# Performance work log

Measured on AMD Instinct MI355X. Metric: run time of the kernel, lower is better.

Reference implementation:

```python
import jax, jax.numpy as jnp
import numpy as np

# ---- config (mirrors init_kwargs) ----
T = 1024          # num tokens (one causal sequence)
H = 1024          # hidden_size
NQ, NK, D = 16, 4, 64   # q heads, kv heads, head_dim (GQA)
I_DENSE = 4096    # dense FFN intermediate
I_MOE = 512       # expert FFN intermediate
E, K = 8, 2       # num_experts, top_k
EPS = 1e-6
THETA = 10000.0


def setup_inputs() -> dict:
    key = jax.random.key(0)
    ks = jax.random.split(key, 20)
    rn = lambda k, shp: (jax.random.normal(k, shp, dtype=jnp.float32) * 0.02)
    QKV = (NQ + 2 * NK) * D
    return {
        "hidden_states": jax.random.normal(ks[0], (T, H), dtype=jnp.float32),
        "residual": jax.random.normal(ks[1], (T, H), dtype=jnp.float32),
        "positions": jnp.arange(T, dtype=jnp.int32),
        "ln0_w": jnp.ones((H,), jnp.float32),
        "pa0_w": jnp.ones((H,), jnp.float32),
        "ln1_w": jnp.ones((H,), jnp.float32),
        "pa1_w": jnp.ones((H,), jnp.float32),
        # attention weights (stored [in, out] so x @ W)
        "qkv0_w": rn(ks[2], (H, QKV)),
        "o0_w": rn(ks[3], (NQ * D, H)),
        "qkv1_w": rn(ks[4], (H, QKV)),
        "o1_w": rn(ks[5], (NQ * D, H)),
        # dense MLPs (merged gate_up: first half gate, second half up)
        "gu0_w": rn(ks[6], (H, 2 * I_DENSE)),
        "dn0_w": rn(ks[7], (I_DENSE, H)),
        "gu1_w": rn(ks[8], (H, 2 * I_DENSE)),
        "dn1_w": rn(ks[9], (I_DENSE, H)),
        # MoE: router gate + per-expert SwiGLU weights
        "gate_w": rn(ks[10], (H, E)),
        "w13": rn(ks[11], (E, H, 2 * I_MOE)),
        "w2": rn(ks[12], (E, I_MOE, H)),
    }


def _rmsnorm(x, w):
    v = jnp.mean(jnp.square(x.astype(jnp.float32)), axis=-1, keepdims=True)
    return (x.astype(jnp.float32) * jax.lax.rsqrt(v + EPS)).astype(x.dtype) * w


def _add_rmsnorm(x, res, w):
    # sglang fused add + RMSNorm: residual <- x + residual; out <- rmsnorm(residual)
    res = x + res
    return _rmsnorm(res, w), res


def _rope(pos, x):
    # neox-style rotary over full head_dim; x: [T, n_heads, D]
    half = D // 2
    inv_freq = 1.0 / (THETA ** (jnp.arange(half, dtype=jnp.float32) / half))
    f = pos.astype(jnp.float32)[:, None] * inv_freq            # [T, half]
    cos, sin = jnp.cos(f)[:, None, :], jnp.sin(f)[:, None, :]  # [T, 1, half]
    x1, x2 = x[..., :half], x[..., half:]
    return jnp.concatenate([x1 * cos - x2 * sin, x2 * cos + x1 * sin], axis=-1)


def _attention(pos, x, qkv_w, o_w):
    qkv = x @ qkv_w
    q = qkv[:, : NQ * D].reshape(T, NQ, D)
    k = qkv[:, NQ * D : (NQ + NK) * D].reshape(T, NK, D)
    v = qkv[:, (NQ + NK) * D :].reshape(T, NK, D)
    q, k = _rope(pos, q), _rope(pos, k)
    g = NQ // NK
    qg = q.reshape(T, NK, g, D)
    scores = jnp.einsum("tkgd,skd->kgts", qg, k) * (D ** -0.5)  # [NK,g,T,T]
    causal = jnp.tril(jnp.ones((T, T), bool))
    scores = jnp.where(causal, scores, jnp.float32(-1e30))
    p = jax.nn.softmax(scores, axis=-1)
    o = jnp.einsum("kgts,skd->tkgd", p, v).reshape(T, NQ * D)
    return o @ o_w


def _dense_mlp(x, gu_w, dn_w):
    gu = x @ gu_w
    h = jax.nn.silu(gu[:, :I_DENSE]) * gu[:, I_DENSE:]  # SiluAndMul
    return h @ dn_w


def _moe(x, gate_w, w13, w2):
    # router in fp32 (router_dtype == 'float32'), softmax, top-k, no renormalize
    logits = x.astype(jnp.float32) @ gate_w.astype(jnp.float32)  # [T, E]
    probs = jax.nn.softmax(logits, axis=-1)
    topw, topi = jax.lax.top_k(probs, K)                         # [T, K]
    rows = jnp.arange(x.shape[0])[:, None]
    combine = jnp.zeros((x.shape[0], E), jnp.float32).at[rows, topi].set(topw)
    combine = combine.astype(x.dtype)
    out = jnp.zeros_like(x)
    for e in range(E):  # fixed small expert count: grouped-GEMM reference
        g = x @ w13[e]
        h = jax.nn.silu(g[:, :I_MOE]) * g[:, I_MOE:]
        out = out + combine[:, e : e + 1] * (h @ w2[e])
    return out


def reference(hidden_states, residual, positions, ln0_w, pa0_w, ln1_w, pa1_w,
              qkv0_w, o0_w, qkv1_w, o1_w, gu0_w, dn0_w, gu1_w, dn1_w,
              gate_w, w13, w2):
    h, r = _add_rmsnorm(hidden_states, residual, ln0_w)
    h = _attention(positions, h, qkv0_w, o0_w)
    h, r = _add_rmsnorm(h, r, pa0_w)
    shortcut = _moe(h, gate_w, w13, w2)      # MoE runs on the shortcut branch
    h = _dense_mlp(h, gu0_w, dn0_w)
    h, r = _add_rmsnorm(h, r, ln1_w)
    h = _attention(positions, h, qkv1_w, o1_w)
    h, r = _add_rmsnorm(h, r, pa1_w)
    h = _dense_mlp(h, gu1_w, dn1_w)
    h = h + shortcut                          # combine shortcut MoE output
    return h, r
```

## Files before the change

kernel.cpp:

```cpp
#include <hip/hip_runtime.h>
#include <math.h>

namespace {

constexpr int kT = 1024;
constexpr int kH = 1024;
constexpr int kNQ = 16;
constexpr int kNKV = 4;
constexpr int kD = 64;
constexpr int kQKV = (kNQ + 2 * kNKV) * kD;
constexpr int kIDense = 4096;
constexpr int kIMoe = 512;
constexpr int kE = 8;
constexpr float kEps = 1e-6f;
constexpr long kTH = (long)kT * kH;

typedef __attribute__((ext_vector_type(8))) short short8;
typedef __attribute__((ext_vector_type(4))) float f32x4;

__device__ __forceinline__ ushort f2bf(float f) {
    union { float f; uint32_t u; } v; v.f = f;
    uint32_t r = (v.u + 0x7fffu + ((v.u >> 16) & 1u)) >> 16;
    return (ushort)r;
}
__device__ __forceinline__ void gload16(const void* g, void* l) {
    __builtin_amdgcn_global_load_lds(
        (const __attribute__((address_space(1))) void*)g,
        (__attribute__((address_space(3))) void*)l, 16, 0, 0);
}

__global__ __launch_bounds__(256) void add_rmsnorm_kernel(
    const float* __restrict__ xP, int nparts, const float* __restrict__ res,
    const float* __restrict__ w, float* __restrict__ h32,
    ushort* __restrict__ h16, float* __restrict__ r_out)
{
    __shared__ float red[4];
    const int t = blockIdx.x;
    const int i = threadIdx.x;
    const size_t base = (size_t)t * kH;
    float4 s = reinterpret_cast<const float4*>(res + base)[i];
    for (int p = 0; p < nparts; p++) {
        float4 a = reinterpret_cast<const float4*>(xP + p * kTH + base)[i];
        s.x += a.x; s.y += a.y; s.z += a.z; s.w += a.w;
    }
    reinterpret_cast<float4*>(r_out + base)[i] = s;
    float ss = s.x * s.x + s.y * s.y + s.z * s.z + s.w * s.w;
    #pragma unroll
    for (int off = 32; off > 0; off >>= 1) ss += __shfl_down(ss, off);
    if ((i & 63) == 0) red[i >> 6] = ss;
    __syncthreads();
    const float tot = red[0] + red[1] + red[2] + red[3];
    const float inv = rsqrtf(tot * (1.0f / kH) + kEps);
    float4 wv = reinterpret_cast<const float4*>(w)[i];
    float4 o = make_float4(s.x * inv * wv.x, s.y * inv * wv.y,
                           s.z * inv * wv.z, s.w * inv * wv.w);
    reinterpret_cast<float4*>(h32 + base)[i] = o;
    ushort4 u;
    u.x = f2bf(o.x); u.y = f2bf(o.y); u.z = f2bf(o.z); u.w = f2bf(o.w);
    reinterpret_cast<ushort4*>(h16 + base)[i] = u;
}

__global__ __launch_bounds__(256) void transpose_bf16_kernel(
    const float* __restrict__ W, ushort* __restrict__ WT,
    int R, int Cn, int ld_w, long w_z_stride, long wt_z_stride)
{
    __shared__ float tile[64 * 65];
    const int z = blockIdx.z;
    const float* Wz = W + (size_t)z * w_z_stride;
    ushort* WTz = WT + (size_t)z * wt_z_stride;
    const int r0 = blockIdx.y * 64;
    const int c0 = blockIdx.x * 64;
    const int tid = threadIdx.x;
    const int lr = tid >> 4;
    const int lc = (tid & 15) * 4;
    #pragma unroll
    for (int p = 0; p < 4; p++) {
        const int row = p * 16 + lr;
        float4 v = *reinterpret_cast<const float4*>(
            &Wz[(size_t)(r0 + row) * ld_w + c0 + lc]);
        tile[row * 65 + lc + 0] = v.x;
        tile[row * 65 + lc + 1] = v.y;
        tile[row * 65 + lc + 2] = v.z;
        tile[row * 65 + lc + 3] = v.w;
    }
    __syncthreads();
    const int ocl = tid >> 2;
    const int q = tid & 3;
    ushort u[16];
    #pragma unroll
    for (int e = 0; e < 16; e++)
        u[e] = f2bf(tile[(q * 16 + e) * 65 + ocl]);
    ushort* dst = &WTz[(size_t)(c0 + ocl) * R + r0 + q * 16];
    *reinterpret_cast<short8*>(dst) = *reinterpret_cast<short8*>(&u[0]);
    *reinterpret_cast<short8*>(dst + 8) = *reinterpret_cast<short8*>(&u[8]);
}

template <bool GATED>
__global__ __launch_bounds__(256) void mgemm_kernel(
    const ushort* __restrict__ A, const ushort* __restrict__ B,
    float* __restrict__ Cf, ushort* __restrict__ C16,
    const float* __restrict__ scale,
    int lda, int ldb, int ldc, int kc,
    int gate_off_rows, long b_z_stride, int c_z_col, int k_z_off,
    int scale_stride, long c_fstride)
{
    __shared__ __align__(16) ushort As[64 * 64];
    __shared__ __align__(16) ushort Bs[64 * 64];
    __shared__ __align__(16) ushort Us[GATED ? 64 * 64 : 8];

    const int z = blockIdx.z;
    const int gy = gridDim.y;
    const int nf = gridDim.x * gy;
    const int fid = blockIdx.x + gridDim.x * blockIdx.y;
    const int qq = nf >> 3;
    const int id2 = (fid & 7) * qq + (fid >> 3);
    const int m0 = (id2 % gy) * 64;
    const int n0 = (id2 / gy) * 64;

    const int tid = threadIdx.x;
    const ushort* Bz = B + (size_t)z * b_z_stride;
    const int k0 = z * k_z_off;

    const int arow = tid >> 3;
    const int achk = tid & 7;

    const int lane = tid & 63;
    const int wave = tid >> 6;
    const int wr = (wave >> 1) * 32;
    const int wc = (wave & 1) * 32;
    const int lrow = lane & 15;
    const int lg = lane >> 4;

    f32x4 accg[2][2] = {};
    f32x4 accu[2][2] = {};

    for (int kk0 = 0; kk0 < kc; kk0 += 64) {
        const int kbase = k0 + kk0;
        #pragma unroll
        for (int c = 0; c < 2; c++) {
            const int row = c * 32 + arow;
            const int cs = (achk + (row & 7)) & 7;
            gload16(A + (size_t)(m0 + row) * lda + kbase + cs * 8,
                    (char*)As + c * 4096 + tid * 16);
            gload16(Bz + (size_t)(n0 + row) * ldb + kbase + cs * 8,
                    (char*)Bs + c * 4096 + tid * 16);
            if constexpr (GATED)
                gload16(Bz + (size_t)(gate_off_rows + n0 + row) * ldb + kbase + cs * 8,
                        (char*)Us + c * 4096 + tid * 16);
        }
        __syncthreads();

        short8 af[2][2], bfr[2][2];
        #pragma unroll
        for (int mf = 0; mf < 2; mf++)
            #pragma unroll
            for (int kk = 0; kk < 2; kk++) {
                const int r = wr + mf * 16 + lrow;
                const int sl = ((kk * 4 + lg) - (r & 7)) & 7;
                af[mf][kk] = *reinterpret_cast<const short8*>(
                    (const char*)As + r * 128 + sl * 16);
            }
        #pragma unroll
        for (int nf2 = 0; nf2 < 2; nf2++)
            #pragma unroll
            for (int kk = 0; kk < 2; kk++) {
                const int n = wc + nf2 * 16 + lrow;
                const int sl = ((kk * 4 + lg) - (n & 7)) & 7;
                bfr[nf2][kk] = *reinterpret_cast<const short8*>(
                    (const char*)Bs + n * 128 + sl * 16);
            }
        #pragma unroll
        for (int mf = 0; mf < 2; mf++)
            #pragma unroll
            for (int nf2 = 0; nf2 < 2; nf2++)
                #pragma unroll
                for (int kk = 0; kk < 2; kk++)
                    accg[mf][nf2] = __builtin_amdgcn_mfma_f32_16x16x32_bf16(
                        af[mf][kk], bfr[nf2][kk], accg[mf][nf2], 0, 0, 0);
        if constexpr (GATED) {
            short8 uf[2][2];
            #pragma unroll
            for (int nf2 = 0; nf2 < 2; nf2++)
                #pragma unroll
                for (int kk = 0; kk < 2; kk++) {
                    const int n = wc + nf2 * 16 + lrow;
                    const int sl = ((kk * 4 + lg) - (n & 7)) & 7;
                    uf[nf2][kk] = *reinterpret_cast<const short8*>(
                        (const char*)Us + n * 128 + sl * 16);
                }
            #pragma unroll
            for (int mf = 0; mf < 2; mf++)
                #pragma unroll
                for (int nf2 = 0; nf2 < 2; nf2++)
                    #pragma unroll
                    for (int kk = 0; kk < 2; kk++)
                        accu[mf][nf2] = __builtin_amdgcn_mfma_f32_16x16x32_bf16(
                            af[mf][kk], uf[nf2][kk], accu[mf][nf2], 0, 0, 0);
        }
        __syncthreads();
    }

    const int r4 = (lane >> 4) * 4;
    const int cl = lane & 15;
    const int ccol = z * c_z_col;
    float* Cfz = Cf ? Cf + (size_t)z * c_fstride : nullptr;
    #pragma unroll
    for (int mf = 0; mf < 2; mf++) {
        #pragma unroll
        for (int nf2 = 0; nf2 < 2; nf2++) {
            #pragma unroll
            for (int j = 0; j < 4; j++) {
                const int row = m0 + wr + mf * 16 + r4 + j;
                const int col = ccol + n0 + wc + nf2 * 16 + cl;
                if constexpr (GATED) {
                    const float g = accg[mf][nf2][j];
                    const float u = accu[mf][nf2][j];
                    const float sv =
                        scale ? scale[(size_t)row * scale_stride + z] : 1.0f;
                    const float h = (g / (1.0f + __expf(-g))) * u * sv;
                    C16[(size_t)row * ldc + col] = f2bf(h);
                } else {
                    Cfz[(size_t)row * ldc + col] = accg[mf][nf2][j];
                }
            }
        }
    }
}

__global__ __launch_bounds__(256) void rope_pack_kernel(
    const float* __restrict__ qkv, const int* __restrict__ positions,
    ushort* __restrict__ Qb, ushort* __restrict__ Kb)
{
    const int t = blockIdx.x;
    const float pos = (float)positions[t];
    for (int item = threadIdx.x; item < (kNQ + kNKV) * 32; item += 256) {
        const int head = item >> 5;
        const int i = item & 31;
        const float inv_freq = powf(10000.0f, -(float)i * (1.0f / 32.0f));
        const float f = pos * inv_freq;
        float sv, cv;
        sincosf(f, &sv, &cv);
        const size_t off = (size_t)t * kQKV + head * kD;
        const float x1 = qkv[off + i];
        const float x2 = qkv[off + 32 + i];
        const float r1 = x1 * cv - x2 * sv;
        const float r2 = x2 * cv + x1 * sv;
        if (head < kNQ) {
            ushort* q = Qb + ((size_t)head * kT + t) * kD;
            q[i] = f2bf(r1 * 0.125f);
            q[i + 32] = f2bf(r2 * 0.125f);
        } else {
            ushort* k = Kb + ((size_t)(head - kNQ) * kT + t) * kD;
            k[i] = f2bf(r1);
            k[i + 32] = f2bf(r2);
        }
    }
}

__global__ __launch_bounds__(64) void gate_topk_kernel(
    const float* __restrict__ h, const float* __restrict__ gate_w,
    float* __restrict__ combine)
{
    const int t = blockIdx.x;
    const int lane = threadIdx.x;
    float acc[kE] = {};
    for (int i = lane; i < kH; i += 64) {
        const float xv = h[(size_t)t * kH + i];
        const float* gw = gate_w + (size_t)i * kE;
        #pragma unroll
        for (int e = 0; e < kE; e++) acc[e] += xv * gw[e];
    }
    #pragma unroll
    for (int e = 0; e < kE; e++) {
        #pragma unroll
        for (int off = 32; off > 0; off >>= 1) acc[e] += __shfl_down(acc[e], off);
    }
    if (lane == 0) {
        float mx = acc[0];
        #pragma unroll
        for (int e = 1; e < kE; e++) mx = fmaxf(mx, acc[e]);
        float p[kE];
        float s = 0.0f;
        #pragma unroll
        for (int e = 0; e < kE; e++) { p[e] = expf(acc[e] - mx); s += p[e]; }
        const float invs = 1.0f / s;
        #pragma unroll
        for (int e = 0; e < kE; e++) p[e] *= invs;
        int i1 = 0;
        #pragma unroll
        for (int e = 1; e < kE; e++) if (p[e] > p[i1]) i1 = e;
        int i2 = (i1 == 0) ? 1 : 0;
        #pragma unroll
        for (int e = 0; e < kE; e++) if (e != i1 && p[e] > p[i2]) i2 = e;
        float outv[kE];
        #pragma unroll
        for (int e = 0; e < kE; e++) outv[e] = 0.0f;
        outv[i1] = p[i1];
        outv[i2] = p[i2];
        #pragma unroll
        for (int e = 0; e < kE; e++) combine[(size_t)t * kE + e] = outv[e];
    }
}

__global__ __launch_bounds__(256) void attn_mfma_kernel(
    const ushort* __restrict__ Qb, const ushort* __restrict__ Kb,
    const ushort* __restrict__ Vt, ushort* __restrict__ attn_o)
{
    __shared__ __align__(16) ushort Qs[64 * 64];
    __shared__ __align__(16) ushort Ks[64 * 64];
    __shared__ __align__(16) ushort Vs[64 * 64];
    __shared__ __align__(16) ushort Ps[64 * 64];
    const int tid = threadIdx.x;
    const int qb = blockIdx.x * 64;
    const int hq = blockIdx.y;
    const int kvh = hq >> 2;
    const int lane = tid & 63;
    const int wave = tid >> 6;
    const int lrow = lane & 15;
    const int g = lane >> 4;
    const int srow = tid >> 3;
    const int sx = tid & 7;
    const ushort* Qg = Qb + ((size_t)hq * kT + qb) * kD;
    const ushort* Kg = Kb + (size_t)kvh * kT * kD;
    const ushort* Vg = Vt + (size_t)kvh * kD * kT;
    const int xr = (lrow & 7) << 4;

    #pragma unroll
    for (int c = 0; c < 2; c++) {
        const int row = c * 32 + srow;
        gload16(Qg + (size_t)row * kD + ((sx ^ (row & 7)) * 8),
                (char*)Qs + c * 4096 + tid * 16);
    }
    __syncthreads();
    short8 qf[2];
    #pragma unroll
    for (int kk = 0; kk < 2; kk++)
        qf[kk] = *reinterpret_cast<const short8*>(
            (const char*)Qs + (16 * wave + lrow) * 128 + ((kk * 64 + g * 16) ^ xr));

    f32x4 oacc[4] = {};
    float mrow = -1e30f, lsum = 0.0f;

    for (int s0 = 0; s0 <= qb; s0 += 64) {
        __syncthreads();
        #pragma unroll
        for (int c = 0; c < 2; c++) {
            const int row = c * 32 + srow;
            gload16(Kg + (size_t)(s0 + row) * kD + ((sx ^ (row & 7)) * 8),
                    (char*)Ks + c * 4096 + tid * 16);
            gload16(Vg + (size_t)row * kT + s0 + ((sx ^ (row & 7)) * 8),
                    (char*)Vs + c * 4096 + tid * 16);
        }
        __syncthreads();

        f32x4 sacc[4] = {};
        #pragma unroll
        for (int nf = 0; nf < 4; nf++) {
            #pragma unroll
            for (int kk = 0; kk < 2; kk++) {
                short8 kf = *reinterpret_cast<const short8*>(
                    (const char*)Ks + (nf * 16 + lrow) * 128 + ((kk * 64 + g * 16) ^ xr));
                sacc[nf] = __builtin_amdgcn_mfma_f32_16x16x32_bf16(
                    kf, qf[kk], sacc[nf], 0, 0, 0);
            }
        }

        const bool diag = (s0 == qb);
        float pv[16];
        float mloc = -1e30f;
        #pragma unroll
        for (int nf = 0; nf < 4; nf++)
            #pragma unroll
            for (int j = 0; j < 4; j++) {
                float s = sacc[nf][j];
                if (diag && (nf * 16 + g * 4 + j > 16 * wave + lrow)) s = -1e30f;
                pv[nf * 4 + j] = s;
                mloc = fmaxf(mloc, s);
            }
        mloc = fmaxf(mloc, __shfl_xor(mloc, 16));
        mloc = fmaxf(mloc, __shfl_xor(mloc, 32));
        const float mnew = fmaxf(mrow, mloc);
        const float alpha = __expf(mrow - mnew);
        float psum = 0.0f;
        #pragma unroll
        for (int j = 0; j < 16; j++) { pv[j] = __expf(pv[j] - mnew); psum += pv[j]; }
        psum += __shfl_xor(psum, 16);
        psum += __shfl_xor(psum, 32);
        lsum = lsum * alpha + psum;
        mrow = mnew;

        const int prow = 16 * wave + lrow;
        #pragma unroll
        for (int nf = 0; nf < 4; nf++)
            #pragma unroll
            for (int jp = 0; jp < 2; jp++) {
                uint32_t pk = (uint32_t)f2bf(pv[nf * 4 + jp * 2]) |
                              ((uint32_t)f2bf(pv[nf * 4 + jp * 2 + 1]) << 16);
                *reinterpret_cast<uint32_t*>(
                    (char*)Ps + prow * 128 + ((nf * 32 + g * 8 + jp * 4) ^ xr)) = pk;
            }

        float aj[4];
        #pragma unroll
        for (int j = 0; j < 4; j++) aj[j] = __shfl(alpha, g * 4 + j);
        #pragma unroll
        for (int nf = 0; nf < 4; nf++)
            #pragma unroll
            for (int j = 0; j < 4; j++) oacc[nf][j] *= aj[j];

        short8 paf[2];
        #pragma unroll
        for (int kk = 0; kk < 2; kk++)
            paf[kk] = *reinterpret_cast<const short8*>(
                (const char*)Ps + prow * 128 + ((kk * 64 + g * 16) ^ xr));
        #pragma unroll
        for (int nf = 0; nf < 4; nf++)
            #pragma unroll
            for (int kk = 0; kk < 2; kk++) {
                short8 vf = *reinterpret_cast<const short8*>(
                    (const char*)Vs + (nf * 16 + lrow) * 128 + ((kk * 64 + g * 16) ^ xr));
                oacc[nf] = __builtin_amdgcn_mfma_f32_16x16x32_bf16(
                    paf[kk], vf, oacc[nf], 0, 0, 0);
            }
    }

    float lj[4];
    #pragma unroll
    for (int j = 0; j < 4; j++) lj[j] = 1.0f / __shfl(lsum, g * 4 + j);
    #pragma unroll
    for (int nf = 0; nf < 4; nf++)
        #pragma unroll
        for (int j = 0; j < 4; j++) {
            const int trow = qb + 16 * wave + g * 4 + j;
            attn_o[(size_t)trow * (kNQ * kD) + hq * kD + nf * 16 + lrow] =
                f2bf(oacc[nf][j] * lj[j]);
        }
}

__global__ __launch_bounds__(256) void final_out_kernel(
    const float* __restrict__ mlpP, const float* __restrict__ scP,
    const float* __restrict__ r, float* __restrict__ out)
{
    const int i = blockIdx.x * 256 + threadIdx.x;
    float4 s = make_float4(0.f, 0.f, 0.f, 0.f);
    #pragma unroll
    for (int p = 0; p < 4; p++) {
        float4 a = reinterpret_cast<const float4*>(mlpP + p * kTH)[i];
        float4 b = reinterpret_cast<const float4*>(scP + p * kTH)[i];
        s.x += a.x + b.x; s.y += a.y + b.y; s.z += a.z + b.z; s.w += a.w + b.w;
    }
    reinterpret_cast<float4*>(out)[i] = s;
    reinterpret_cast<float4*>(out + kTH)[i] =
        reinterpret_cast<const float4*>(r)[i];
}

}

extern "C" void kernel_launch(void* const* d_in, const int* in_sizes, int n_in,
                              void* d_out, int out_size, void* d_ws, size_t ws_size,
                              hipStream_t stream) {
    (void)in_sizes; (void)n_in; (void)out_size; (void)ws_size;
    const float* hidden   = (const float*)d_in[0];
    const float* residual = (const float*)d_in[1];
    const int*   positions= (const int*)d_in[2];
    const float* ln0_w    = (const float*)d_in[3];
    const float* pa0_w    = (const float*)d_in[4];
    const float* ln1_w    = (const float*)d_in[5];
    const float* pa1_w    = (const float*)d_in[6];
    const float* qkv0_w   = (const float*)d_in[7];
    const float* o0_w     = (const float*)d_in[8];
    const float* qkv1_w   = (const float*)d_in[9];
    const float* o1_w     = (const float*)d_in[10];
    const float* gu0_w    = (const float*)d_in[11];
    const float* dn0_w    = (const float*)d_in[12];
    const float* gu1_w    = (const float*)d_in[13];
    const float* dn1_w    = (const float*)d_in[14];
    const float* gate_w   = (const float*)d_in[15];
    const float* w13      = (const float*)d_in[16];
    const float* w2       = (const float*)d_in[17];
    float* out_h = (float*)d_out;

    char* wsb = (char*)d_ws;
    float*  r_buf   = (float*)(wsb + (0ull  << 20));
    float*  h32     = (float*)(wsb + (4ull  << 20));
    float*  t0P     = (float*)(wsb + (8ull  << 20));
    float*  cb_buf  = (float*)(wsb + (8ull  << 20));
    float*  scP     = (float*)(wsb + (24ull << 20));
    ushort* h16     = (ushort*)(wsb + (40ull << 20));
    ushort* ao16    = (ushort*)(wsb + (42ull << 20));
    float*  qkv_buf = (float*)(wsb + (44ull << 20));
    ushort* he16    = (ushort*)(wsb + (44ull << 20));
    ushort* wT      = (ushort*)(wsb + (52ull << 20));
    ushort* Qb      = (ushort*)(wsb + (62ull << 20));
    ushort* Kb      = (ushort*)(wsb + (64ull << 20));
    ushort* VtG     = (ushort*)(wsb + (65ull << 20));

    auto transp = [&](const float* W, int R, int Cn, int nz, long zs_in, long zs_out) {
        transpose_bf16_kernel<<<dim3(Cn / 64, R / 64, nz), 256, 0, stream>>>(
            W, wT, R, Cn, Cn, zs_in, zs_out);
    };
    auto gemm_f32 = [&](const ushort* A, float* C, int N, int lda_,
                        int ldb_, int ldc_, int nz, int kc, int kzoff) {
        mgemm_kernel<false><<<dim3(N / 64, kT / 64, nz), 256, 0, stream>>>(
            A, wT, C, nullptr, nullptr, lda_, ldb_, ldc_, kc,
            0, 0, 0, kzoff, 0, kTH);
    };
    auto attention = [&](const float* qkv_w, const float* o_w) {
        transp(qkv_w, kH, kQKV, 1, 0, 0);
        mgemm_kernel<false><<<dim3(kQKV / 64, kT / 64, 1), 256, 0, stream>>>(
            h16, wT, qkv_buf, nullptr, nullptr, kH, kH, kQKV, kH,
            0, 0, 0, 0, 0, 0);
        rope_pack_kernel<<<kT, 256, 0, stream>>>(qkv_buf, positions, Qb, Kb);
        transpose_bf16_kernel<<<dim3(1, kT / 64, kNKV), 256, 0, stream>>>(
            qkv_buf + (kNQ + kNKV) * kD, VtG, kT, kD, kQKV, kD, (long)kD * kT);
        attn_mfma_kernel<<<dim3(kT / 64, kNQ), 256, 0, stream>>>(Qb, Kb, VtG, ao16);
        transp(o_w, kNQ * kD, kH, 1, 0, 0);
        gemm_f32(ao16, t0P, kH, kNQ * kD, kNQ * kD, kH, 2, 512, 512);
    };
    auto dense_mlp = [&](const float* gu_w, const float* dn_w) {
        transp(gu_w, kH, 2 * kIDense, 1, 0, 0);
        mgemm_kernel<true><<<dim3(kIDense / 64, kT / 64, 1), 256, 0, stream>>>(
            h16, wT, nullptr, he16, nullptr, kH, kH, kIDense, kH,
            kIDense, 0, 0, 0, 0, 0);
        transp(dn_w, kIDense, kH, 1, 0, 0);
        gemm_f32(he16, t0P, kH, kIDense, kIDense, kH, 4, 1024, 1024);
    };

    add_rmsnorm_kernel<<<kT, 256, 0, stream>>>(hidden, 1, residual, ln0_w, h32, h16, r_buf);
    attention(qkv0_w, o0_w);
    add_rmsnorm_kernel<<<kT, 256, 0, stream>>>(t0P, 2, r_buf, pa0_w, h32, h16, r_buf);
    gate_topk_kernel<<<kT, 64, 0, stream>>>(h32, gate_w, cb_buf);
    transp(w13, kH, 2 * kIMoe, kE, (long)kH * 2 * kIMoe, (long)kH * 2 * kIMoe);
    mgemm_kernel<true><<<dim3(kIMoe / 64, kT / 64, kE), 256, 0, stream>>>(
        h16, wT, nullptr, he16, cb_buf, kH, kH, kIDense, kH,
        kIMoe, (long)kH * 2 * kIMoe, kIMoe, 0, kE, 0);
    transp(w2, kE * kIMoe, kH, 1, 0, 0);
    gemm_f32(he16, scP, kH, kIDense, kIDense, kH, 4, 1024, 1024);
    dense_mlp(gu0_w, dn0_w);
    add_rmsnorm_kernel<<<kT, 256, 0, stream>>>(t0P, 4, r_buf, ln1_w, h32, h16, r_buf);
    attention(qkv1_w, o1_w);
    add_rmsnorm_kernel<<<kT, 256, 0, stream>>>(t0P, 2, r_buf, pa1_w, h32, h16, r_buf);
    dense_mlp(gu1_w, dn1_w);
    final_out_kernel<<<(kT * kH / 4) / 256, 256, 0, stream>>>(t0P, scP, r_buf, out_h);
}
```

Measured before the change: 345.0 us.

## Split causal attention KV range across two blocks and merge partials

The attention kernel now runs on a z=2 grid. Each block handles half of the causal KV tiles for its query block and writes unnormalized fp32 partial outputs plus row max and sum. It also schedules the heaviest query blocks first through a reversed block index. A new merge kernel combines the two partials with log-sum-exp rescaling and writes the bf16 output. This doubles the block count (256 to 512) to fill more CUs and evens out causal imbalance, at the cost of an extra kernel launch and fp32 partial traffic.

After: 335.8 us. -2.7%, faster.

```diff
diff --git a/kernel.cpp b/kernel.cpp
--- a/kernel.cpp
+++ b/kernel.cpp
@@ -304,16 +304,34 @@
 
 __global__ __launch_bounds__(256) void attn_mfma_kernel(
     const ushort* __restrict__ Qb, const ushort* __restrict__ Kb,
-    const ushort* __restrict__ Vt, ushort* __restrict__ attn_o)
+    const ushort* __restrict__ Vt, float* __restrict__ Opart,
+    float* __restrict__ mlpart)
 {
     __shared__ __align__(16) ushort Qs[64 * 64];
     __shared__ __align__(16) ushort Ks[64 * 64];
     __shared__ __align__(16) ushort Vs[64 * 64];
     __shared__ __align__(16) ushort Ps[64 * 64];
     const int tid = threadIdx.x;
-    const int qb = blockIdx.x * 64;
+    const int qbi = (int)gridDim.x - 1 - blockIdx.x;
+    const int qb = qbi * 64;
     const int hq = blockIdx.y;
+    const int zp = blockIdx.z;
     const int kvh = hq >> 2;
+
+    const int nt = qbi + 1;
+    const int halfc = (nt + 1) >> 1;
+    const int sbeg = zp ? halfc : 0;
+    const int send = zp ? nt : halfc;
+
+    float* Oz = Opart + (((size_t)zp * kNQ + hq) * kT + qb) * kD;
+    float* mlz = mlpart + (((size_t)zp * kNQ + hq) * kT + qb) * 2;
+
+    if (sbeg >= send) {
+        for (int i = tid; i < 64 * kD; i += 256) Oz[(i >> 6) * kD + (i & 63)] = 0.f;
+        for (int i = tid; i < 64; i += 256) { mlz[i * 2] = -1e30f; mlz[i * 2 + 1] = 0.f; }
+        return;
+    }
+
     const int lane = tid & 63;
     const int wave = tid >> 6;
     const int lrow = lane & 15;
@@ -341,7 +359,8 @@
     f32x4 oacc[4] = {};
     float mrow = -1e30f, lsum = 0.0f;
 
-    for (int s0 = 0; s0 <= qb; s0 += 64) {
+    for (int ti = sbeg; ti < send; ++ti) {
+        const int s0 = ti * 64;
         __syncthreads();
         #pragma unroll
         for (int c = 0; c < 2; c++) {
@@ -424,17 +443,41 @@
             }
     }
 
-    float lj[4];
-    #pragma unroll
-    for (int j = 0; j < 4; j++) lj[j] = 1.0f / __shfl(lsum, g * 4 + j);
     #pragma unroll
     for (int nf = 0; nf < 4; nf++)
         #pragma unroll
-        for (int j = 0; j < 4; j++) {
-            const int trow = qb + 16 * wave + g * 4 + j;
-            attn_o[(size_t)trow * (kNQ * kD) + hq * kD + nf * 16 + lrow] =
-                f2bf(oacc[nf][j] * lj[j]);
-        }
+        for (int j = 0; j < 4; j++)
+            Oz[(16 * wave + g * 4 + j) * kD + nf * 16 + lrow] = oacc[nf][j];
+    if (g == 0) {
+        mlz[(16 * wave + lrow) * 2 + 0] = mrow;
+        mlz[(16 * wave + lrow) * 2 + 1] = lsum;
+    }
+}
+
+__global__ __launch_bounds__(256) void attn_merge_kernel(
+    const float* __restrict__ Opart, const float* __restrict__ mlpart,
+    ushort* __restrict__ attn_o)
+{
+    const int trow = blockIdx.x;
+    const int tid = threadIdx.x;
+    const int head = tid >> 4;
+    const int c4 = (tid & 15) * 4;
+    const size_t i0 = ((size_t)head * kT + trow);
+    const size_t i1 = (((size_t)kNQ + head) * kT + trow);
+    const float m0 = mlpart[i0 * 2], l0 = mlpart[i0 * 2 + 1];
+    const float m1 = mlpart[i1 * 2], l1 = mlpart[i1 * 2 + 1];
+    const float m = fmaxf(m0, m1);
+    const float e0 = __expf(m0 - m), e1 = __expf(m1 - m);
+    const float inv = 1.0f / (l0 * e0 + l1 * e1);
+    float4 a = *reinterpret_cast<const float4*>(&Opart[i0 * kD + c4]);
+    float4 b = *reinterpret_cast<const float4*>(&Opart[i1 * kD + c4]);
+    ushort4 u;
+    u.x = f2bf((a.x * e0 + b.x * e1) * inv);
+    u.y = f2bf((a.y * e0 + b.y * e1) * inv);
+    u.z = f2bf((a.z * e0 + b.z * e1) * inv);
+    u.w = f2bf((a.w * e0 + b.w * e1) * inv);
+    *reinterpret_cast<ushort4*>(
+        &attn_o[(size_t)trow * (kNQ * kD) + head * kD + c4]) = u;
 }
 
 __global__ __launch_bounds__(256) void final_out_kernel(
@@ -485,11 +528,13 @@
     float*  h32     = (float*)(wsb + (4ull  << 20));
     float*  t0P     = (float*)(wsb + (8ull  << 20));
     float*  cb_buf  = (float*)(wsb + (8ull  << 20));
+    float*  Opart   = (float*)(wsb + (16ull << 20));
     float*  scP     = (float*)(wsb + (24ull << 20));
     ushort* h16     = (ushort*)(wsb + (40ull << 20));
     ushort* ao16    = (ushort*)(wsb + (42ull << 20));
     float*  qkv_buf = (float*)(wsb + (44ull << 20));
     ushort* he16    = (ushort*)(wsb + (44ull << 20));
+    float*  ml_buf  = (float*)(wsb + (50ull << 20));
     ushort* wT      = (ushort*)(wsb + (52ull << 20));
     ushort* Qb      = (ushort*)(wsb + (62ull << 20));
     ushort* Kb      = (ushort*)(wsb + (64ull << 20));
@@ -513,7 +558,9 @@
         rope_pack_kernel<<<kT, 256, 0, stream>>>(qkv_buf, positions, Qb, Kb);
         transpose_bf16_kernel<<<dim3(1, kT / 64, kNKV), 256, 0, stream>>>(
             qkv_buf + (kNQ + kNKV) * kD, VtG, kT, kD, kQKV, kD, (long)kD * kT);
-        attn_mfma_kernel<<<dim3(kT / 64, kNQ), 256, 0, stream>>>(Qb, Kb, VtG, ao16);
+        attn_mfma_kernel<<<dim3(kT / 64, kNQ, 2), 256, 0, stream>>>(
+            Qb, Kb, VtG, Opart, ml_buf);
+        attn_merge_kernel<<<kT, 256, 0, stream>>>(Opart, ml_buf, ao16);
         transp(o_w, kNQ * kD, kH, 1, 0, 0);
         gemm_f32(ao16, t0P, kH, kNQ * kD, kNQ * kD, kH, 2, 512, 512);
     };
```
